# Kernel tuning notes

Measured on AMD Instinct MI355X. Metric: run time of the kernel, lower is better.

Reference implementation:

```python
import jax, jax.numpy as jnp
import numpy as np

B, T, C, H = 2, 512, 64, 64  # batch, seq (<= block_size), n_embd, head_size


def setup_inputs() -> dict:
    key = jax.random.key(0)
    ks = jax.random.split(key, 9)
    p = lambda k, sh: jax.random.normal(k, sh, jnp.float32) * 0.02
    return {
        "x": jax.random.normal(ks[0], (B, T, C), jnp.float32),
        "pos_emb": jax.random.normal(ks[1], (T, C), jnp.float32),
        "pos_dist_emb": jax.random.normal(ks[2], (B, T, T, 2 * C), jnp.float32),
        # GeluFeedForward(4c -> c -> 1): Linear(4c, c) -> GELU -> Linear(c, 1)
        "W1": p(ks[3], (4 * C, C)),
        "b1": p(ks[4], (C,)),
        "W2": p(ks[5], (C, 1)),
        "b2": p(ks[6], (1,)),
        # value projection Linear(c, head_size)
        "Wv": p(ks[7], (C, H)),
        "bv": p(ks[8], (H,)),
    }


def reference(x, pos_emb, pos_dist_emb, W1, b1, W2, b2, Wv, bv):
    b, t, c = x.shape
    x1 = x + pos_emb  # (b,t,c)
    # cat([k, q, pos_dist], -1) @ W1 == k@W1[:c] + q@W1[c:2c] + pd@W1[2c:]
    # (avoids materializing the (b,t,t,4c) repeat+cat tensor; same math)
    W1k, W1q, W1p = W1[:c], W1[c:2 * c], W1[2 * c:]
    kp = x1 @ W1k                 # (b,t,c): key side, varies over pair axis 2
    qp = x1 @ W1q                 # (b,t,c): query side, varies over pair axis 1
    pp = pos_dist_emb @ W1p       # (b,t,t,c)
    h = jax.nn.gelu(qp[:, :, None, :] + kp[:, None, :, :] + pp + b1,
                    approximate=False)          # (b,t,t,c)
    wei = ((h @ W2)[..., 0] + b2[0]) * (c ** -0.5)  # (b,t,t)
    causal = jnp.tril(jnp.ones((t, t), bool))
    wei = jnp.where(causal, wei, -jnp.inf)
    wei = jax.nn.softmax(wei, axis=-1)          # (b,t,t); dropout p=0
    v = x @ Wv + bv                             # (b,t,H)
    return wei @ v                              # (b,t,H)
```

## Files before the change

kernel.cpp:

```cpp
#include <hip/hip_runtime.h>
#include <math.h>

#define BB 2
#define TT 512
#define CC 64
#define HH 64
#define KK 128
#define JT 64

typedef __attribute__((ext_vector_type(8))) short short8;
typedef __attribute__((ext_vector_type(4))) float float4v;

__device__ inline unsigned short f2bf(float f) {
    unsigned int u = __float_as_uint(f);
    u = (u + 0x7FFFu + ((u >> 16) & 1u)) >> 16;
    return (unsigned short)u;
}

__global__ __launch_bounds__(64) void prep_kernel(
    const float* __restrict__ x, const float* __restrict__ pos_emb,
    const float* __restrict__ W1, const float* __restrict__ b1,
    const float* __restrict__ Wv, const float* __restrict__ bv,
    float* __restrict__ kp, float* __restrict__ qpb, float* __restrict__ v,
    unsigned short* __restrict__ Wpt)
{
    if (blockIdx.x >= BB * TT) {
        int base = (blockIdx.x - BB * TT) * 256 + threadIdx.x;
#pragma unroll
        for (int q = 0; q < 4; ++q) {
            int o  = base + q * 64;
            int e  = o & 7;
            int mm = (o >> 3) & 15;
            int kg = (o >> 7) & 3;
            int kt = (o >> 9) & 3;
            int nt = (o >> 11) & 3;
            int k = kt * 32 + kg * 8 + e;
            int c = nt * 16 + mm;
            Wpt[o] = f2bf(W1[(2 * CC + k) * CC + c]);
        }
        return;
    }

    const int row = blockIdx.x;
    const int t = row & (TT - 1);
    const int c = threadIdx.x;
    __shared__ float xs[CC], x1s[CC];
    float xv = x[row * CC + c];
    xs[c] = xv;
    x1s[c] = xv + pos_emb[t * CC + c];
    __syncthreads();
    float ak = 0.f, aq = 0.f, av = 0.f;
#pragma unroll 8
    for (int k = 0; k < CC; ++k) {
        ak = fmaf(x1s[k], W1[k * CC + c], ak);
        aq = fmaf(x1s[k], W1[(CC + k) * CC + c], aq);
        av = fmaf(xs[k], Wv[k * HH + c], av);
    }
    kp[row * CC + c] = ak;
    qpb[row * CC + c] = aq + b1[c];
    v[row * HH + c] = av + bv[c];
}

__global__ __launch_bounds__(256, 4) void wei_kernel(
    const float* __restrict__ pd, const unsigned short* __restrict__ Wpt,
    const float* __restrict__ W2, const float* __restrict__ b2,
    const float* __restrict__ kp, const float* __restrict__ qpb,
    float* __restrict__ wei)
{
    const int i = blockIdx.y;
    const int b = blockIdx.z;
    const int j0 = blockIdx.x * JT;
    if (j0 > i) return;

    __shared__ unsigned short Alds[JT * KK];

    const int tid  = threadIdx.x;
    const int wave = tid >> 6;
    const int lane = tid & 63;
    const int m    = lane & 15;
    const int kg   = lane >> 4;

    float w2v[4], qv[4];
#pragma unroll
    for (int nt = 0; nt < 4; ++nt) {
        int c = nt * 16 + m;
        w2v[nt] = W2[c];
        qv[nt]  = qpb[((size_t)b * TT + i) * CC + c];
    }
    const float b2v = b2[0];

    {
        const float4* __restrict__ p4 =
            (const float4*)(pd + (((size_t)b * TT + i) * TT + j0) * KK);
#pragma unroll
        for (int it = 0; it < 8; ++it) {
            int f = it * 256 + tid;
            float4 val = p4[f];
            int j  = f >> 5;
            int kq = f & 31;
            uint2 u;
            u.x = (unsigned)f2bf(val.x) | ((unsigned)f2bf(val.y) << 16);
            u.y = (unsigned)f2bf(val.z) | ((unsigned)f2bf(val.w) << 16);
            *(uint2*)&Alds[j * KK + ((kq * 4) ^ ((j & 7) << 3))] = u;
        }
    }
    __syncthreads();

    float4v acc[4] = {{0.f,0.f,0.f,0.f},{0.f,0.f,0.f,0.f},
                      {0.f,0.f,0.f,0.f},{0.f,0.f,0.f,0.f}};
    const int arow  = wave * 16 + m;
    const int abase = arow * KK;
    const int a7    = (arow & 7) << 3;
#pragma unroll
    for (int kt = 0; kt < 4; ++kt) {
        short8 a = *(const short8*)&Alds[abase + ((kt * 32 + kg * 8) ^ a7)];
#pragma unroll
        for (int nt = 0; nt < 4; ++nt) {
            short8 bf = *(const short8*)&Wpt[((nt * 4 + kt) * 64 + lane) * 8];
            acc[nt] = __builtin_amdgcn_mfma_f32_16x16x32_bf16(a, bf, acc[nt], 0, 0, 0);
        }
    }

#pragma unroll
    for (int r = 0; r < 4; ++r) {
        const int j = j0 + wave * 16 + kg * 4 + r;
        float s = 0.f;
#pragma unroll
        for (int nt = 0; nt < 4; ++nt) {
            float tv = acc[nt][r] + qv[nt]
                     + kp[((size_t)b * TT + j) * CC + nt * 16 + m];
            float g = 0.5f * tv * (1.f + erff(tv * 0.70710678118654752f));
            s = fmaf(g, w2v[nt], s);
        }
#pragma unroll
        for (int off = 1; off < 16; off <<= 1) s += __shfl_xor(s, off);
        if (m == r && j <= i)
            wei[((size_t)b * TT + i) * TT + j] = (s + b2v) * 0.125f;
    }
}

__device__ inline float wave_reduce_max(float m) {
#pragma unroll
    for (int off = 32; off > 0; off >>= 1) m = fmaxf(m, __shfl_down(m, off));
    return m;
}
__device__ inline float wave_reduce_sum(float s) {
#pragma unroll
    for (int off = 32; off > 0; off >>= 1) s += __shfl_down(s, off);
    return s;
}

__global__ __launch_bounds__(256) void out_kernel(
    const float* __restrict__ wei, const float* __restrict__ v,
    float* __restrict__ out)
{
    const int i = blockIdx.x;
    const int b = blockIdx.y;
    const int tid = threadIdx.x;
    const int wv = tid >> 6;
    const int lane = tid & 63;
    const int n = i + 1;

    __shared__ float p[TT];
    __shared__ float red[4];
    __shared__ float4v part[4][16];

    const float* wrow = wei + ((size_t)b * TT + i) * TT;

    float mx = -1e30f;
    for (int jj = tid; jj < n; jj += 256) {
        float w = wrow[jj];
        p[jj] = w;
        mx = fmaxf(mx, w);
    }
    mx = wave_reduce_max(mx);
    if (lane == 0) red[wv] = mx;
    __syncthreads();
    const float M = fmaxf(fmaxf(red[0], red[1]), fmaxf(red[2], red[3]));
    __syncthreads();

    float s = 0.f;
    for (int jj = tid; jj < n; jj += 256) {
        float e = __expf(p[jj] - M);
        p[jj] = e;
        s += e;
    }
    s = wave_reduce_sum(s);
    if (lane == 0) red[wv] = s;
    __syncthreads();
    const float S = red[0] + red[1] + red[2] + red[3];
    const float inv = 1.f / S;

    const int c4 = lane & 15;
    const int jr = lane >> 4;
    const float4v* v4 = (const float4v*)(v + (size_t)b * TT * HH);
    float4v acc = {0.f, 0.f, 0.f, 0.f};
    for (int base = wv * 4; base < n; base += 16) {
        int j = base + jr;
        float pj = (j < n) ? p[j] : 0.f;
        int jc = (j < n) ? j : 0;
        float4v vv = v4[jc * 16 + c4];
        acc += vv * pj;
    }
#pragma unroll
    for (int off = 16; off <= 32; off <<= 1) {
        float4v t;
        t[0] = __shfl_xor(acc[0], off);
        t[1] = __shfl_xor(acc[1], off);
        t[2] = __shfl_xor(acc[2], off);
        t[3] = __shfl_xor(acc[3], off);
        acc += t;
    }
    if (jr == 0) part[wv][c4] = acc;
    __syncthreads();
    if (tid < 16) {
        float4v r = (part[0][tid] + part[1][tid] + part[2][tid] + part[3][tid]) * inv;
        *((float4v*)(out + ((size_t)b * TT + i) * HH) + tid) = r;
    }
}

extern "C" void kernel_launch(void* const* d_in, const int* in_sizes, int n_in,
                              void* d_out, int out_size, void* d_ws, size_t ws_size,
                              hipStream_t stream)
{
    const float* x       = (const float*)d_in[0];
    const float* pos_emb = (const float*)d_in[1];
    const float* pd      = (const float*)d_in[2];
    const float* W1      = (const float*)d_in[3];
    const float* b1      = (const float*)d_in[4];
    const float* W2      = (const float*)d_in[5];
    const float* b2      = (const float*)d_in[6];
    const float* Wv      = (const float*)d_in[7];
    const float* bv      = (const float*)d_in[8];
    float* out = (float*)d_out;

    float* ws = (float*)d_ws;
    unsigned short* Wpt = (unsigned short*)ws;
    float* kp  = ws + 4096;
    float* qpb = ws + 4096 + 65536;
    float* v   = ws + 4096 + 131072;
    float* wei = ws + 4096 + 196608;

    prep_kernel<<<dim3(BB * TT + 32), dim3(64), 0, stream>>>(x, pos_emb, W1, b1, Wv, bv, kp, qpb, v, Wpt);
    wei_kernel<<<dim3(TT / JT, TT, BB), dim3(256), 0, stream>>>(pd, Wpt, W2, b2, kp, qpb, wei);
    out_kernel<<<dim3(TT, BB), dim3(256), 0, stream>>>(wei, v, out);
}
```

Baseline: 386.7 us.

## Fuse pairwise score computation with softmax and value aggregation per query row

Merges the score kernel and the softmax/output kernel into one kernel with one block per query row. The block loops over causal key tiles, keeps scores in shared memory, and stages the bf16 weight tile in LDS. This removes the global wei round trip and a launch, and skips loading pd rows above the diagonal. In exchange there are far fewer blocks and each block does serial per-tile work, which reduces parallelism and adds load imbalance across rows.

```diff
diff --git a/kernel.cpp b/kernel.cpp
--- a/kernel.cpp
+++ b/kernel.cpp
@@ -61,25 +61,33 @@
     v[row * HH + c] = av + bv[c];
 }
 
-__global__ __launch_bounds__(256, 4) void wei_kernel(
+__global__ __launch_bounds__(256, 4) void fused_kernel(
     const float* __restrict__ pd, const unsigned short* __restrict__ Wpt,
     const float* __restrict__ W2, const float* __restrict__ b2,
     const float* __restrict__ kp, const float* __restrict__ qpb,
-    float* __restrict__ wei)
+    const float* __restrict__ v, float* __restrict__ out)
 {
-    const int i = blockIdx.y;
-    const int b = blockIdx.z;
-    const int j0 = blockIdx.x * JT;
-    if (j0 > i) return;
-
-    __shared__ unsigned short Alds[JT * KK];
-
+    const int i = blockIdx.x;
+    const int b = blockIdx.y;
     const int tid  = threadIdx.x;
     const int wave = tid >> 6;
     const int lane = tid & 63;
     const int m    = lane & 15;
     const int kg   = lane >> 4;
 
+    __shared__ unsigned short Alds[JT * KK];
+    __shared__ unsigned short Blds[16 * 64 * 8];
+    __shared__ float p[TT];
+    __shared__ float red[4];
+    __shared__ float4v part[4][16];
+
+    {
+        const uint4* __restrict__ src = (const uint4*)Wpt;
+        uint4* dst = (uint4*)Blds;
+#pragma unroll
+        for (int f = 0; f < 4; ++f) dst[f * 256 + tid] = src[f * 256 + tid];
+    }
+
     float w2v[4], qv[4];
 #pragma unroll
     for (int nt = 0; nt < 4; ++nt) {
@@ -89,92 +97,78 @@
     }
     const float b2v = b2[0];
 
-    {
-        const float4* __restrict__ p4 =
-            (const float4*)(pd + (((size_t)b * TT + i) * TT + j0) * KK);
-#pragma unroll
-        for (int it = 0; it < 8; ++it) {
-            int f = it * 256 + tid;
-            float4 val = p4[f];
-            int j  = f >> 5;
-            int kq = f & 31;
-            uint2 u;
-            u.x = (unsigned)f2bf(val.x) | ((unsigned)f2bf(val.y) << 16);
-            u.y = (unsigned)f2bf(val.z) | ((unsigned)f2bf(val.w) << 16);
-            *(uint2*)&Alds[j * KK + ((kq * 4) ^ ((j & 7) << 3))] = u;
-        }
-    }
-    __syncthreads();
-
-    float4v acc[4] = {{0.f,0.f,0.f,0.f},{0.f,0.f,0.f,0.f},
-                      {0.f,0.f,0.f,0.f},{0.f,0.f,0.f,0.f}};
-    const int arow  = wave * 16 + m;
-    const int abase = arow * KK;
-    const int a7    = (arow & 7) << 3;
-#pragma unroll
-    for (int kt = 0; kt < 4; ++kt) {
-        short8 a = *(const short8*)&Alds[abase + ((kt * 32 + kg * 8) ^ a7)];
-#pragma unroll
-        for (int nt = 0; nt < 4; ++nt) {
-            short8 bf = *(const short8*)&Wpt[((nt * 4 + kt) * 64 + lane) * 8];
-            acc[nt] = __builtin_amdgcn_mfma_f32_16x16x32_bf16(a, bf, acc[nt], 0, 0, 0);
-        }
-    }
-
-#pragma unroll
-    for (int r = 0; r < 4; ++r) {
-        const int j = j0 + wave * 16 + kg * 4 + r;
-        float s = 0.f;
-#pragma unroll
-        for (int nt = 0; nt < 4; ++nt) {
-            float tv = acc[nt][r] + qv[nt]
-                     + kp[((size_t)b * TT + j) * CC + nt * 16 + m];
-            float g = 0.5f * tv * (1.f + erff(tv * 0.70710678118654752f));
-            s = fmaf(g, w2v[nt], s);
-        }
-#pragma unroll
-        for (int off = 1; off < 16; off <<= 1) s += __shfl_xor(s, off);
-        if (m == r && j <= i)
-            wei[((size_t)b * TT + i) * TT + j] = (s + b2v) * 0.125f;
-    }
-}
-
-__device__ inline float wave_reduce_max(float m) {
-#pragma unroll
-    for (int off = 32; off > 0; off >>= 1) m = fmaxf(m, __shfl_down(m, off));
-    return m;
-}
-__device__ inline float wave_reduce_sum(float s) {
-#pragma unroll
-    for (int off = 32; off > 0; off >>= 1) s += __shfl_down(s, off);
-    return s;
-}
-
-__global__ __launch_bounds__(256) void out_kernel(
-    const float* __restrict__ wei, const float* __restrict__ v,
-    float* __restrict__ out)
-{
-    const int i = blockIdx.x;
-    const int b = blockIdx.y;
-    const int tid = threadIdx.x;
-    const int wv = tid >> 6;
-    const int lane = tid & 63;
+    const float* __restrict__ kprow = kp + (size_t)b * TT * CC;
+    const int ntiles = (i >> 6) + 1;
+
+    for (int jt = 0; jt < ntiles; ++jt) {
+        const int j0 = jt * JT;
+
+        float4v acc[4];
+#pragma unroll
+        for (int r = 0; r < 4; ++r) {
+            int j = j0 + wave * 16 + kg * 4 + r;
+#pragma unroll
+            for (int nt = 0; nt < 4; ++nt)
+                acc[nt][r] = kprow[j * CC + nt * 16 + m] + qv[nt];
+        }
+
+        __syncthreads();
+
+        {
+            const float4* __restrict__ p4 =
+                (const float4*)(pd + (((size_t)b * TT + i) * TT + j0) * KK);
+#pragma unroll
+            for (int it = 0; it < 8; ++it) {
+                int f = it * 256 + tid;
+                int j  = f >> 5;
+                int kq = f & 31;
+                if (j0 + j <= i) {
+                    float4 val = p4[f];
+                    uint2 u;
+                    u.x = (unsigned)f2bf(val.x) | ((unsigned)f2bf(val.y) << 16);
+                    u.y = (unsigned)f2bf(val.z) | ((unsigned)f2bf(val.w) << 16);
+                    *(uint2*)&Alds[j * KK + ((kq * 4) ^ ((j & 7) << 3))] = u;
+                }
+            }
+        }
+        __syncthreads();
+
+        const int arow  = wave * 16 + m;
+        const int abase = arow * KK;
+        const int a7    = (arow & 7) << 3;
+#pragma unroll
+        for (int kt = 0; kt < 4; ++kt) {
+            short8 a = *(const short8*)&Alds[abase + ((kt * 32 + kg * 8) ^ a7)];
+#pragma unroll
+            for (int nt = 0; nt < 4; ++nt) {
+                short8 bf = *(const short8*)&Blds[((nt * 4 + kt) * 64 + lane) * 8];
+                acc[nt] = __builtin_amdgcn_mfma_f32_16x16x32_bf16(a, bf, acc[nt], 0, 0, 0);
+            }
+        }
+
+#pragma unroll
+        for (int r = 0; r < 4; ++r) {
+            float s = 0.f;
+#pragma unroll
+            for (int nt = 0; nt < 4; ++nt) {
+                float tv = acc[nt][r];
+                float g = 0.5f * tv * (1.f + erff(tv * 0.70710678118654752f));
+                s = fmaf(g, w2v[nt], s);
+            }
+#pragma unroll
+            for (int off = 1; off < 16; off <<= 1) s += __shfl_xor(s, off);
+            const int j = j0 + wave * 16 + kg * 4 + r;
+            if (m == r && j <= i) p[j] = (s + b2v) * 0.125f;
+        }
+    }
+    __syncthreads();
+
     const int n = i + 1;
-
-    __shared__ float p[TT];
-    __shared__ float red[4];
-    __shared__ float4v part[4][16];
-
-    const float* wrow = wei + ((size_t)b * TT + i) * TT;
-
     float mx = -1e30f;
-    for (int jj = tid; jj < n; jj += 256) {
-        float w = wrow[jj];
-        p[jj] = w;
-        mx = fmaxf(mx, w);
-    }
-    mx = wave_reduce_max(mx);
-    if (lane == 0) red[wv] = mx;
+    for (int jj = tid; jj < n; jj += 256) mx = fmaxf(mx, p[jj]);
+#pragma unroll
+    for (int off = 32; off > 0; off >>= 1) mx = fmaxf(mx, __shfl_down(mx, off));
+    if (lane == 0) red[wave] = mx;
     __syncthreads();
     const float M = fmaxf(fmaxf(red[0], red[1]), fmaxf(red[2], red[3]));
     __syncthreads();
@@ -185,8 +179,9 @@
         p[jj] = e;
         s += e;
     }
-    s = wave_reduce_sum(s);
-    if (lane == 0) red[wv] = s;
+#pragma unroll
+    for (int off = 32; off > 0; off >>= 1) s += __shfl_down(s, off);
+    if (lane == 0) red[wave] = s;
     __syncthreads();
     const float S = red[0] + red[1] + red[2] + red[3];
     const float inv = 1.f / S;
@@ -195,7 +190,7 @@
     const int jr = lane >> 4;
     const float4v* v4 = (const float4v*)(v + (size_t)b * TT * HH);
     float4v acc = {0.f, 0.f, 0.f, 0.f};
-    for (int base = wv * 4; base < n; base += 16) {
+    for (int base = wave * 4; base < n; base += 16) {
         int j = base + jr;
         float pj = (j < n) ? p[j] : 0.f;
         int jc = (j < n) ? j : 0;
@@ -211,7 +206,7 @@
         t[3] = __shfl_xor(acc[3], off);
         acc += t;
     }
-    if (jr == 0) part[wv][c4] = acc;
+    if (jr == 0) part[wave][c4] = acc;
     __syncthreads();
     if (tid < 16) {
         float4v r = (part[0][tid] + part[1][tid] + part[2][tid] + part[3][tid]) * inv;
@@ -239,9 +234,7 @@
     float* kp  = ws + 4096;
     float* qpb = ws + 4096 + 65536;
     float* v   = ws + 4096 + 131072;
-    float* wei = ws + 4096 + 196608;
 
     prep_kernel<<<dim3(BB * TT + 32), dim3(64), 0, stream>>>(x, pos_emb, W1, b1, Wv, bv, kp, qpb, v, Wpt);
-    wei_kernel<<<dim3(TT / JT, TT, BB), dim3(256), 0, stream>>>(pd, Wpt, W2, b2, kp, qpb, wei);
-    out_kernel<<<dim3(TT, BB), dim3(256), 0, stream>>>(wei, v, out);
-}
+    fused_kernel<<<dim3(TT, BB), dim3(256), 0, stream>>>(pd, Wpt, W2, b2, kp, qpb, v, out);
+}
```

New measurement: 376.6 us. -2.6%, faster.
